# Kernel optimization log

Measured on AMD Instinct MI355X. Metric: run time of the kernel, lower is better.

The kernel has to match this reference:

```python
import jax, jax.numpy as jnp
import numpy as np

H = 4
HD = 32
C = 128
NU = 40000
NI = 40000
E = 200000


def _linear(x, W, b):
    # torch Linear: y = x @ W.T + b, W is [out, in]
    return x @ W.T + b


def _counts_in(query, sorted_keys):
    l = jnp.searchsorted(sorted_keys, query, side='left')
    r = jnp.searchsorted(sorted_keys, query, side='right')
    return (r - l).astype(jnp.float32)


def _segment_softmax(scores, seg, n):
    # scores: [E, H], seg: [E] destination ids
    m = jax.ops.segment_max(scores, seg, num_segments=n)
    m = jnp.where(jnp.isfinite(m), m, 0.0)
    e = jnp.exp(scores - m[seg])
    z = jax.ops.segment_sum(e, seg, num_segments=n)
    return e / z[seg]


def _deg_count(idx, n):
    return jnp.zeros((n,), jnp.float32).at[idx].add(1.0)


def _layernorm(x):
    mu = x.mean(-1, keepdims=True)
    var = ((x - mu) ** 2).mean(-1, keepdims=True)
    return (x - mu) / jnp.sqrt(var + 1e-5)


def _relation(x_src, x_dst, src, dst, t_src, t_dst,
              Wq, bq, Wk, bk, Wv, bv, Wo, bo,
              head_bias, beta, tau_raw, gamma, delta,
              counts, recips, n_dst):
    Q = _linear(x_dst, Wq, bq).reshape(-1, H, HD)
    K = _linear(x_src, Wk, bk).reshape(-1, H, HD)
    V = _linear(x_src, Wv, bv).reshape(-1, H, HD)
    Qe, Ke, Ve = Q[dst], K[src], V[src]                      # [E, H, HD]
    scores = (Qe * Ke).sum(-1) / jnp.sqrt(jnp.float32(HD))   # [E, H]
    scores = scores + head_bias
    dt = jnp.abs(t_dst[dst] - t_src[src]) + 1e-6
    tau = jax.nn.softplus(tau_raw) + 1e-6
    scores = scores + (-jnp.log1p(dt / tau))[:, None] * beta
    scores = scores + jnp.log1p(counts)[:, None] * gamma
    scores = scores + recips[:, None] * delta
    w = _segment_softmax(scores, dst, n_dst)                 # [E, H]
    out_e = (Ve * w[:, :, None]).reshape(-1, C)
    out_e = _linear(out_e, Wo, bo)
    return jnp.zeros((n_dst, C), x_dst.dtype).at[dst].add(out_e)


def setup_inputs() -> dict:
    key = jax.random.key(0)
    ks = jax.random.split(key, 20)
    inp = {
        'x_user': jax.random.normal(ks[0], (NU, C), jnp.float32),
        'x_item': jax.random.normal(ks[1], (NI, C), jnp.float32),
        't_user': jax.random.uniform(ks[2], (NU,), jnp.float32) * 100.0,
        't_item': jax.random.uniform(ks[3], (NI,), jnp.float32) * 100.0,
        'edge_index_ui': jax.random.randint(ks[4], (2, E), 0, NU, jnp.int32),
        'edge_index_iu': jax.random.randint(ks[5], (2, E), 0, NI, jnp.int32),
        'Wq': jax.random.normal(ks[6], (C, C), jnp.float32) * 0.05,
        'bq': jax.random.normal(ks[7], (C,), jnp.float32) * 0.05,
        'Wk': jax.random.normal(ks[8], (C, C), jnp.float32) * 0.05,
        'bk': jax.random.normal(ks[9], (C,), jnp.float32) * 0.05,
        'Wv': jax.random.normal(ks[10], (C, C), jnp.float32) * 0.05,
        'bv': jax.random.normal(ks[11], (C,), jnp.float32) * 0.05,
        'Wo': jax.random.normal(ks[12], (C, C), jnp.float32) * 0.05,
        'bo': jax.random.normal(ks[13], (C,), jnp.float32) * 0.05,
        'rel_head_bias': jax.random.normal(ks[14], (2, H), jnp.float32) * 0.1,
        'time_beta': jax.random.normal(ks[15], (2, H), jnp.float32) * 0.1,
        'time_tau_raw': jax.random.normal(ks[16], (2,), jnp.float32),
        'gamma_multirel': jax.random.normal(ks[17], (2, H), jnp.float32) * 0.1,
        'delta_recip': jax.random.normal(ks[18], (2, H), jnp.float32) * 0.1,
    }
    return inp


def reference(x_user, x_item, t_user, t_item, edge_index_ui, edge_index_iu,
              Wq, bq, Wk, bk, Wv, bv, Wo, bo,
              rel_head_bias, time_beta, time_tau_raw, gamma_multirel, delta_recip):
    su, du = edge_index_ui[0], edge_index_ui[1]   # user -> item
    si, di = edge_index_iu[0], edge_index_iu[1]   # item -> user
    # multirel counts (pair multiplicity - 1) and reciprocity flags, per relation
    pid_ui = su * NI + du            # (user,item) pair ids (fits int32: NU*NI < 2^31)
    pid_iu = si * NU + di            # (item,user) pair ids
    rev_for_ui = di * NI + si        # reversed pairs of iu edges in (user,item) space
    rev_for_iu = du * NU + su        # reversed pairs of ui edges in (item,user) space
    counts_ui = _counts_in(pid_ui, jnp.sort(pid_ui)) - 1.0
    counts_iu = _counts_in(pid_iu, jnp.sort(pid_iu)) - 1.0
    recips_ui = (_counts_in(pid_ui, jnp.sort(rev_for_ui)) > 0).astype(jnp.float32)
    recips_iu = (_counts_in(pid_iu, jnp.sort(rev_for_iu)) > 0).astype(jnp.float32)

    out_item = _relation(x_user, x_item, su, du, t_user, t_item,
                         Wq, bq, Wk, bk, Wv, bv, Wo, bo,
                         rel_head_bias[0], time_beta[0], time_tau_raw[0],
                         gamma_multirel[0], delta_recip[0], counts_ui, recips_ui, NI)
    out_user = _relation(x_item, x_user, si, di, t_item, t_user,
                         Wq, bq, Wk, bk, Wv, bv, Wo, bo,
                         rel_head_bias[1], time_beta[1], time_tau_raw[1],
                         gamma_multirel[1], delta_recip[1], counts_iu, recips_iu, NU)
    # degree centrality bias: total (in + out) degree added to every channel
    deg_user = _deg_count(su, NU) + _deg_count(di, NU)
    deg_item = _deg_count(du, NI) + _deg_count(si, NI)
    out_user = out_user + deg_user[:, None]
    out_item = out_item + deg_item[:, None]
    return _layernorm(out_user + x_user), _layernorm(out_item + x_item)
```

## Files before the change

kernel.cpp:

```cpp
#include <hip/hip_runtime.h>
#include <math.h>

constexpr int kH  = 4;
constexpr int kHD = 32;
constexpr int kC  = 128;
constexpr int kNU = 40000;
constexpr int kNI = 40000;
constexpr int kE  = 200000;
constexpr int kNT = kNU + kNI;
constexpr int kSB = (kNT + 1023) / 1024;
constexpr int kTilesPerSide = kNU / 16;
constexpr int kTiles = kNT / 16;
constexpr int kGemmBlocks  = 768;
constexpr int kTableBlocks = 1536;
constexpr int kFusedBlocks = 2304;

#define DEV_INLINE __device__ __forceinline__

typedef short bf16x8 __attribute__((ext_vector_type(8)));
typedef float f32x4  __attribute__((ext_vector_type(4)));
typedef uint32_t u32x4 __attribute__((ext_vector_type(4)));
typedef unsigned long long u64;

DEV_INLINE unsigned short f2bf(float f) {
  uint32_t u = __float_as_uint(f);
  u += 0x7fffu + ((u >> 16) & 1u);
  return (unsigned short)(u >> 16);
}

DEV_INLINE float bflo(uint32_t u) { return __uint_as_float(u << 16); }
DEV_INLINE float bfhi(uint32_t u) { return __uint_as_float(u & 0xffff0000u); }

DEV_INLINE int swz(int row, int elem) {
  return (elem & 7) | (((elem >> 3) ^ (row & 7)) << 3);
}

DEV_INLINE int rpf(const int* __restrict__ rp, const int* __restrict__ boff, int i) {
  return rp[i] + boff[i >> 10];
}

__global__ void cast4w_bf16(const float* __restrict__ w0, const float* __restrict__ w1,
                            const float* __restrict__ w2, const float* __restrict__ w3,
                            unsigned short* __restrict__ o0, unsigned short* __restrict__ o1,
                            unsigned short* __restrict__ o2, unsigned short* __restrict__ o3) {
  int i = blockIdx.x * blockDim.x + threadIdx.x;
  int m = i >> 12, j = i & 4095;
  const float* in = (m == 0) ? w0 : (m == 1) ? w1 : (m == 2) ? w2 : w3;
  unsigned short* out = (m == 0) ? o0 : (m == 1) ? o1 : (m == 2) ? o2 : o3;
  float4 v = ((const float4*)in)[j];
  ushort4 o = {f2bf(v.x), f2bf(v.y), f2bf(v.z), f2bf(v.w)};
  ((ushort4*)out)[j] = o;
}

__global__ __launch_bounds__(256, 3) void qkv_build(
    const float* __restrict__ Xu, const float* __restrict__ Xi,
    const unsigned short* __restrict__ Wq, const unsigned short* __restrict__ Wk,
    const unsigned short* __restrict__ Wv,
    const float* __restrict__ bq, const float* __restrict__ bk,
    const float* __restrict__ bv,
    unsigned short* __restrict__ Qu, unsigned short* __restrict__ Ku,
    unsigned short* __restrict__ Vu,
    unsigned short* __restrict__ Qi, unsigned short* __restrict__ Ki,
    unsigned short* __restrict__ Vi,
    const int* __restrict__ du, const int* __restrict__ di,
    int* __restrict__ deg_all, int* __restrict__ pos_all) {
  __shared__ unsigned short sx[16 * kC];
  __shared__ unsigned short sr[3 * 16 * kC];
  const int bid = blockIdx.x;
  const int tid = threadIdx.x;

  if (bid % 3 != 1) {
    const int tb = (bid / 3) * 2 + ((bid % 3) ? 1 : 0);
    for (int t = tb * 256 + tid; t < 2 * kE; t += kTableBlocks * 256) {
      if (t < kE) {
        pos_all[t] = atomicAdd(&deg_all[du[t]], 1);
      } else {
        pos_all[t] = atomicAdd(&deg_all[kNI + di[t - kE]], 1);
      }
    }
    return;
  }

  const int gb   = bid / 3;
  const int wave = tid >> 6;
  const int lane = tid & 63;
  const int mr   = lane & 15;
  const int quad = lane >> 4;
  const int ct0  = wave * 2;
  const int srow = tid >> 4;
  const int schk = tid & 15;

  bf16x8 wf[3][2][4];
  {
    const unsigned short* Ws[3] = {Wq, Wk, Wv};
#pragma unroll
    for (int m = 0; m < 3; ++m)
#pragma unroll
      for (int c = 0; c < 2; ++c) {
        const unsigned short* wrow = Ws[m] + (size_t)((ct0 + c) * 16 + mr) * kC + quad * 8;
#pragma unroll
        for (int kc = 0; kc < 4; ++kc) wf[m][c][kc] = *(const bf16x8*)(wrow + kc * 32);
      }
  }

  int tile = gb;
  float4 xa, xb;
  {
    const bool item = tile >= kTilesPerSide;
    const float* X = item ? Xi : Xu;
    const int base = (item ? tile - kTilesPerSide : tile) * 16;
    const float* xr = X + (size_t)(base + srow) * kC + schk * 8;
    xa = ((const float4*)xr)[0];
    xb = ((const float4*)xr)[1];
  }

  for (; tile < kTiles; tile += kGemmBlocks) {
    const bool item = tile >= kTilesPerSide;
    const int base = (item ? tile - kTilesPerSide : tile) * 16;

    {
      bf16x8 p;
      p[0] = (short)f2bf(xa.x); p[1] = (short)f2bf(xa.y);
      p[2] = (short)f2bf(xa.z); p[3] = (short)f2bf(xa.w);
      p[4] = (short)f2bf(xb.x); p[5] = (short)f2bf(xb.y);
      p[6] = (short)f2bf(xb.z); p[7] = (short)f2bf(xb.w);
      *(bf16x8*)(sx + srow * kC + ((schk ^ (srow & 7)) << 3)) = p;
    }
    __syncthreads();

    bf16x8 b[4];
#pragma unroll
    for (int kc = 0; kc < 4; ++kc)
      b[kc] = *(const bf16x8*)(sx + mr * kC + (((quad + kc * 4) ^ (mr & 7)) << 3));

    int ntile = tile + kGemmBlocks;
    if (ntile < kTiles) {
      const bool nit = ntile >= kTilesPerSide;
      const float* X = nit ? Xi : Xu;
      const int nbase = (nit ? ntile - kTilesPerSide : ntile) * 16;
      const float* xr = X + (size_t)(nbase + srow) * kC + schk * 8;
      xa = ((const float4*)xr)[0];
      xb = ((const float4*)xr)[1];
    }

    f32x4 acc[3][2];
#pragma unroll
    for (int m = 0; m < 3; ++m) {
      acc[m][0] = (f32x4){0.f, 0.f, 0.f, 0.f};
      acc[m][1] = (f32x4){0.f, 0.f, 0.f, 0.f};
    }
#pragma unroll
    for (int kc = 0; kc < 4; ++kc)
#pragma unroll
      for (int m = 0; m < 3; ++m)
#pragma unroll
        for (int c = 0; c < 2; ++c)
          acc[m][c] = __builtin_amdgcn_mfma_f32_16x16x32_bf16(wf[m][c][kc], b[kc], acc[m][c], 0, 0, 0);

    const float* bs[3] = {bq, bk, bv};
#pragma unroll
    for (int m = 0; m < 3; ++m)
#pragma unroll
      for (int c = 0; c < 2; ++c) {
        int c0 = (ct0 + c) * 16 + quad * 4;
        float4 bb = *(const float4*)(bs[m] + c0);
        uint2 p;
        p.x = (uint32_t)f2bf(acc[m][c][0] + bb.x) | ((uint32_t)f2bf(acc[m][c][1] + bb.y) << 16);
        p.y = (uint32_t)f2bf(acc[m][c][2] + bb.z) | ((uint32_t)f2bf(acc[m][c][3] + bb.w) << 16);
        *(uint2*)(sr + (m * 16 + mr) * kC + swz(mr, c0)) = p;
      }
    __syncthreads();

    {
      unsigned short* Os[3] = {item ? Qi : Qu, item ? Ki : Ku, item ? Vi : Vu};
      const int el = (schk ^ (srow & 7)) << 3;
#pragma unroll
      for (int m = 0; m < 3; ++m) {
        bf16x8 v = *(const bf16x8*)(sr + (m * 16 + srow) * kC + el);
        *(bf16x8*)(Os[m] + (size_t)(base + srow) * kC + schk * 8) = v;
      }
    }
  }
}

__global__ __launch_bounds__(256) void scan1(const int* __restrict__ in,
                                             int* __restrict__ out,
                                             int* __restrict__ bsum, int n) {
  __shared__ int sh[256];
  const int t = threadIdx.x;
  const int base = blockIdx.x * 1024 + t * 4;
  int4 v = {0, 0, 0, 0};
  if (base + 3 < n) {
    v = *(const int4*)(in + base);
  } else {
    if (base + 0 < n) v.x = in[base + 0];
    if (base + 1 < n) v.y = in[base + 1];
    if (base + 2 < n) v.z = in[base + 2];
    if (base + 3 < n) v.w = in[base + 3];
  }
  int s = v.x + v.y + v.z + v.w;
  sh[t] = s;
  __syncthreads();
  int val = s;
  for (int off = 1; off < 256; off <<= 1) {
    int add = (t >= off) ? sh[t - off] : 0;
    __syncthreads();
    val += add;
    sh[t] = val;
    __syncthreads();
  }
  int excl = val - s;
  if (base + 0 < n) out[base + 0] = excl;
  if (base + 1 < n) out[base + 1] = excl + v.x;
  if (base + 2 < n) out[base + 2] = excl + v.x + v.y;
  if (base + 3 < n) out[base + 3] = excl + v.x + v.y + v.z;
  if (t == 255) bsum[blockIdx.x] = val;
}

__global__ __launch_bounds__(128) void scan2(const int* __restrict__ bsum,
                                             int* __restrict__ boff,
                                             int* __restrict__ rp_tail, int nb) {
  __shared__ int sh[128];
  const int t = threadIdx.x;
  int v = (t < nb) ? bsum[t] : 0;
  sh[t] = v;
  __syncthreads();
  int val = v;
  for (int off = 1; off < 128; off <<= 1) {
    int add = (t >= off) ? sh[t - off] : 0;
    __syncthreads();
    val += add;
    sh[t] = val;
    __syncthreads();
  }
  if (t < nb) boff[t] = val - v;
  if (t == nb - 1) *rp_tail = v;
}

__global__ void scatter_pk(const int* __restrict__ su, const int* __restrict__ du,
                           const int* __restrict__ si, const int* __restrict__ di,
                           const int* __restrict__ rp_all, const int* __restrict__ boff,
                           const int* __restrict__ pos_all,
                           u64* __restrict__ el_all) {
  int t = blockIdx.x * blockDim.x + threadIdx.x;
  if (t >= 2 * kE) return;
  int e, s, dg;
  if (t < kE) { e = t;       s = su[e]; dg = du[e]; }
  else        { e = t - kE;  s = si[e]; dg = kNI + di[e]; }
  el_all[rpf(rp_all, boff, dg) + pos_all[t]] = (u64)(uint32_t)e | ((u64)(uint32_t)s << 32);
}

__global__ void bias_csr(const int* __restrict__ su, const int* __restrict__ du,
                         const int* __restrict__ si, const int* __restrict__ di,
                         const float* __restrict__ t_user, const float* __restrict__ t_item,
                         const int* __restrict__ rp_all, const int* __restrict__ boff,
                         const u64* __restrict__ el_all,
                         const float* __restrict__ hb, const float* __restrict__ beta,
                         const float* __restrict__ taur,
                         const float* __restrict__ gamma, const float* __restrict__ delta,
                         float4* __restrict__ bias_ui, float4* __restrict__ bias_iu) {
  int t = blockIdx.x * blockDim.x + threadIdx.x;
  if (t >= 2 * kE) return;
  const int rel = (t >= kE) ? 1 : 0;
  const int e = rel ? t - kE : t;
  int s, d; float ts, td; int dg, rg;
  if (rel == 0) {
    s = su[e]; d = du[e]; ts = t_user[s]; td = t_item[d];
    dg = d;
    rg = kNI + s;
  } else {
    s = si[e]; d = di[e]; ts = t_item[s]; td = t_user[d];
    dg = kNI + d;
    rg = s;
  }
  int b0 = rpf(rp_all, boff, dg), b1 = rpf(rp_all, boff, dg + 1);
  int cnt = 0;
  for (int p = b0; p < b1; ++p) cnt += ((int)(el_all[p] >> 32) == s);
  int r0 = rpf(rp_all, boff, rg), r1 = rpf(rp_all, boff, rg + 1);
  int rcp = 0;
  for (int p = r0; p < r1; ++p) rcp |= ((int)(el_all[p] >> 32) == d);

  float cntv = (float)(cnt - 1);
  float rec  = (float)rcp;
  float dt   = fabsf(td - ts) + 1e-6f;
  float tau  = log1pf(expf(taur[rel])) + 1e-6f;
  float tterm = -log1pf(dt / tau);
  float lc    = log1pf(cntv);
  const float* hp = hb + rel * kH;
  const float* bp = beta + rel * kH;
  const float* gp = gamma + rel * kH;
  const float* dp = delta + rel * kH;
  const float kL2E = 1.4426950408889634f;
  float4 b;
  b.x = (hp[0] + bp[0] * tterm + gp[0] * lc + dp[0] * rec) * kL2E;
  b.y = (hp[1] + bp[1] * tterm + gp[1] * lc + dp[1] * rec) * kL2E;
  b.z = (hp[2] + bp[2] * tterm + gp[2] * lc + dp[2] * rec) * kL2E;
  b.w = (hp[3] + bp[3] * tterm + gp[3] * lc + dp[3] * rec) * kL2E;
  (rel ? bias_iu : bias_ui)[e] = b;
}

__global__ __launch_bounds__(256) void attn_agg(
    const int* __restrict__ rp_all, const int* __restrict__ boff,
    const u64* __restrict__ el_all,
    const unsigned short* __restrict__ Qi, const unsigned short* __restrict__ Ku,
    const unsigned short* __restrict__ Vu,
    const unsigned short* __restrict__ Qu, const unsigned short* __restrict__ Ki,
    const unsigned short* __restrict__ Vi,
    const float* __restrict__ bias_ui, const float* __restrict__ bias_iu,
    unsigned short* __restrict__ h_ui, unsigned short* __restrict__ h_iu) {
  const int tid = threadIdx.x;
  const int sub = tid & 15;
  const int h   = sub >> 2;
  const int ch0 = h * kHD + (sub & 3) * 8;
  const int g = blockIdx.x * 16 + (tid >> 4);
  if (g >= kNT) return;
  const bool isU = g >= kNI;
  const int n = isU ? g - kNI : g;
  const unsigned short* Q = isU ? Qu : Qi;
  const unsigned short* K = isU ? Ki : Ku;
  const unsigned short* V = isU ? Vi : Vu;
  const float* bias = isU ? bias_iu : bias_ui;
  unsigned short* out = isU ? h_iu : h_ui;

  const int beg = rpf(rp_all, boff, g), end = rpf(rp_all, boff, g + 1);
  const float kScaleL2E = 1.4426950408889634f * 0.17677669529663687f;

  float qf[8];
  {
    u32x4 qv = *(const u32x4*)(Q + (size_t)n * kC + ch0);
#pragma unroll
    for (int w = 0; w < 4; ++w) { qf[2 * w] = bflo(qv[w]); qf[2 * w + 1] = bfhi(qv[w]); }
  }

  float z = 0.f;
  float acc[8] = {0.f, 0.f, 0.f, 0.f, 0.f, 0.f, 0.f, 0.f};

  int e0 = 0, s0 = 0;
  if (beg < end) { u64 pk = el_all[beg]; e0 = (int)pk; s0 = (int)(pk >> 32); }
  u32x4 k0 = *(const u32x4*)(K + (size_t)s0 * kC + ch0);
  u32x4 v0 = *(const u32x4*)(V + (size_t)s0 * kC + ch0);
  float b0 = bias[e0 * 4 + h];

  for (int p = beg; p < end; ++p) {
    int e1 = 0, s1 = 0;
    if (p + 1 < end) { u64 pk = el_all[p + 1]; e1 = (int)pk; s1 = (int)(pk >> 32); }
    u32x4 k1 = *(const u32x4*)(K + (size_t)s1 * kC + ch0);
    u32x4 v1 = *(const u32x4*)(V + (size_t)s1 * kC + ch0);
    float b1 = bias[e1 * 4 + h];

    float d0 = qf[0] * bflo(k0[0]);
    float d1 = qf[1] * bfhi(k0[0]);
    d0 = fmaf(qf[2], bflo(k0[1]), d0);
    d1 = fmaf(qf[3], bfhi(k0[1]), d1);
    d0 = fmaf(qf[4], bflo(k0[2]), d0);
    d1 = fmaf(qf[5], bfhi(k0[2]), d1);
    d0 = fmaf(qf[6], bflo(k0[3]), d0);
    d1 = fmaf(qf[7], bfhi(k0[3]), d1);
    float dsc = d0 + d1;
    dsc += __shfl_xor(dsc, 1);
    dsc += __shfl_xor(dsc, 2);
    float wgt = __builtin_amdgcn_exp2f(fmaf(dsc, kScaleL2E, b0));
    z += wgt;
#pragma unroll
    for (int w = 0; w < 4; ++w) {
      acc[2 * w]     = fmaf(bflo(v0[w]), wgt, acc[2 * w]);
      acc[2 * w + 1] = fmaf(bfhi(v0[w]), wgt, acc[2 * w + 1]);
    }
    k0 = k1; v0 = v1; b0 = b1;
  }

  const float zi = (end > beg) ? 1.0f / z : 0.0f;
  bf16x8 o;
#pragma unroll
  for (int j = 0; j < 8; ++j) o[j] = (short)f2bf(acc[j] * zi);
  *(bf16x8*)(out + (size_t)n * kC + ch0) = o;
}

__global__ __launch_bounds__(256, 4) void wo_ln(
    const unsigned short* __restrict__ Hiu, const unsigned short* __restrict__ Hui,
    const unsigned short* __restrict__ Wo,
    const float* __restrict__ Xu, const float* __restrict__ Xi,
    const int* __restrict__ degU, const int* __restrict__ degI,
    const float* __restrict__ bo, float* __restrict__ out) {
  __shared__ unsigned short sh_h[16 * kC];
  __shared__ float sh_p[64 * 2];
  const int tid  = threadIdx.x;
  const int wave = tid >> 6;
  const int lane = tid & 63;
  const int mr   = lane & 15;
  const int quad = lane >> 4;
  const int ct0  = wave * 2;
  const int srow = tid >> 4;
  const int schk = tid & 15;

  bf16x8 wf[2][4];
#pragma unroll
  for (int c = 0; c < 2; ++c) {
    const unsigned short* wrow = Wo + (size_t)((ct0 + c) * 16 + mr) * kC + quad * 8;
#pragma unroll
    for (int kc = 0; kc < 4; ++kc) wf[c][kc] = *(const bf16x8*)(wrow + kc * 32);
  }
  float4 bb[2];
  bb[0] = *(const float4*)(bo + ct0 * 16 + quad * 4);
  bb[1] = *(const float4*)(bo + (ct0 + 1) * 16 + quad * 4);

  int tile = blockIdx.x;
  bf16x8 hv;
  {
    const bool item = tile >= kTilesPerSide;
    const unsigned short* Hs = item ? Hui : Hiu;
    const int base = (item ? tile - kTilesPerSide : tile) * 16;
    hv = *(const bf16x8*)(Hs + (size_t)(base + srow) * kC + schk * 8);
  }

  for (; tile < kTiles; tile += gridDim.x) {
    const bool item = tile >= kTilesPerSide;
    const int base = (item ? tile - kTilesPerSide : tile) * 16;

    *(bf16x8*)(sh_h + srow * kC + ((schk ^ (srow & 7)) << 3)) = hv;
    __syncthreads();

    bf16x8 b[4];
#pragma unroll
    for (int kc = 0; kc < 4; ++kc)
      b[kc] = *(const bf16x8*)(sh_h + mr * kC + (((quad + kc * 4) ^ (mr & 7)) << 3));

    int ntile = tile + gridDim.x;
    if (ntile < kTiles) {
      const bool nit = ntile >= kTilesPerSide;
      const unsigned short* Hs = nit ? Hui : Hiu;
      const int nbase = (nit ? ntile - kTilesPerSide : ntile) * 16;
      hv = *(const bf16x8*)(Hs + (size_t)(nbase + srow) * kC + schk * 8);
    }

    f32x4 acc[2];
    acc[0] = (f32x4){0.f, 0.f, 0.f, 0.f};
    acc[1] = (f32x4){0.f, 0.f, 0.f, 0.f};
#pragma unroll
    for (int kc = 0; kc < 4; ++kc) {
      acc[0] = __builtin_amdgcn_mfma_f32_16x16x32_bf16(wf[0][kc], b[kc], acc[0], 0, 0, 0);
      acc[1] = __builtin_amdgcn_mfma_f32_16x16x32_bf16(wf[1][kc], b[kc], acc[1], 0, 0, 0);
    }

    const int n = base + mr;
    const float* Xs = item ? Xi : Xu;
    const float fdg = (float)(item ? degI[n] : degU[n]);
    float y[8], s1 = 0.f, s2 = 0.f;
#pragma unroll
    for (int c = 0; c < 2; ++c) {
      int c0 = (ct0 + c) * 16 + quad * 4;
      float4 xv = *(const float4*)(Xs + (size_t)n * kC + c0);
      y[c * 4 + 0] = acc[c][0] + xv.x + fdg * bb[c].x;
      y[c * 4 + 1] = acc[c][1] + xv.y + fdg * bb[c].y;
      y[c * 4 + 2] = acc[c][2] + xv.z + fdg * bb[c].z;
      y[c * 4 + 3] = acc[c][3] + xv.w + fdg * bb[c].w;
#pragma unroll
      for (int j = 0; j < 4; ++j) {
        s1 += y[c * 4 + j];
        s2 += y[c * 4 + j] * y[c * 4 + j];
      }
    }
    s1 += __shfl_xor(s1, 16); s2 += __shfl_xor(s2, 16);
    s1 += __shfl_xor(s1, 32); s2 += __shfl_xor(s2, 32);
    if (quad == 0) {
      sh_p[(wave * 16 + mr) * 2]     = s1;
      sh_p[(wave * 16 + mr) * 2 + 1] = s2;
    }
    __syncthreads();
    float t1 = 0.f, t2 = 0.f;
#pragma unroll
    for (int ww = 0; ww < 4; ++ww) {
      t1 += sh_p[(ww * 16 + mr) * 2];
      t2 += sh_p[(ww * 16 + mr) * 2 + 1];
    }
    float mu   = t1 * (1.0f / 128.0f);
    float var  = t2 * (1.0f / 128.0f) - mu * mu;
    float rstd = rsqrtf(fmaxf(var, 0.0f) + 1e-5f);
    float* op = out + (item ? (size_t)kNU * kC : (size_t)0) + (size_t)n * kC;
#pragma unroll
    for (int c = 0; c < 2; ++c) {
      int c0 = (ct0 + c) * 16 + quad * 4;
      float4 o = {(y[c * 4 + 0] - mu) * rstd, (y[c * 4 + 1] - mu) * rstd,
                  (y[c * 4 + 2] - mu) * rstd, (y[c * 4 + 3] - mu) * rstd};
      *(float4*)(op + c0) = o;
    }
  }
}

extern "C" void kernel_launch(void* const* d_in, const int* in_sizes, int n_in,
                              void* d_out, int out_size, void* d_ws, size_t ws_size,
                              hipStream_t stream) {
  const float* x_user = (const float*)d_in[0];
  const float* x_item = (const float*)d_in[1];
  const float* t_user = (const float*)d_in[2];
  const float* t_item = (const float*)d_in[3];
  const int*   eui    = (const int*)d_in[4];
  const int*   eiu    = (const int*)d_in[5];
  const float* Wq = (const float*)d_in[6];
  const float* bq = (const float*)d_in[7];
  const float* Wk = (const float*)d_in[8];
  const float* bk = (const float*)d_in[9];
  const float* Wv = (const float*)d_in[10];
  const float* bv = (const float*)d_in[11];
  const float* Wo = (const float*)d_in[12];
  const float* bo = (const float*)d_in[13];
  const float* hb    = (const float*)d_in[14];
  const float* beta  = (const float*)d_in[15];
  const float* taur  = (const float*)d_in[16];
  const float* gamma = (const float*)d_in[17];
  const float* delta = (const float*)d_in[18];

  const int* su = eui;       const int* du = eui + kE;
  const int* si = eiu;       const int* di = eiu + kE;

  float* w = (float*)d_ws;
  size_t o = 0;
  unsigned short* qu_b = (unsigned short*)(w + o); o += (size_t)kNU * kC / 2;
  unsigned short* ku_b = (unsigned short*)(w + o); o += (size_t)kNU * kC / 2;
  unsigned short* vu_b = (unsigned short*)(w + o); o += (size_t)kNU * kC / 2;
  unsigned short* qi_b = (unsigned short*)(w + o); o += (size_t)kNI * kC / 2;
  unsigned short* ki_b = (unsigned short*)(w + o); o += (size_t)kNI * kC / 2;
  unsigned short* vi_b = (unsigned short*)(w + o); o += (size_t)kNI * kC / 2;
  unsigned short* h_ui = (unsigned short*)(w + o); o += (size_t)kNI * kC / 2;
  unsigned short* h_iu = (unsigned short*)(w + o); o += (size_t)kNU * kC / 2;
  unsigned short* wq_b = (unsigned short*)(w + o); o += kC * kC / 2;
  unsigned short* wk_b = (unsigned short*)(w + o); o += kC * kC / 2;
  unsigned short* wv_b = (unsigned short*)(w + o); o += kC * kC / 2;
  unsigned short* wo_b = (unsigned short*)(w + o); o += kC * kC / 2;
  float* zero_base = w + o;
  int* deg_all = (int*)(w + o); o += kNT;
  size_t zero_bytes = (size_t)((w + o) - zero_base) * sizeof(float);
  float* bias_ui = w + o; o += (size_t)kE * kH;
  float* bias_iu = w + o; o += (size_t)kE * kH;
  int* rp_all  = (int*)(w + o); o += kNT + 1;
  int* bsum    = (int*)(w + o); o += kSB;
  int* boff    = (int*)(w + o); o += kSB;
  o = (o + 1) & ~(size_t)1;
  u64* el_all  = (u64*)(w + o); o += (size_t)2 * kE * 2;
  int* pos_all = (int*)h_ui;

  hipMemsetAsync(zero_base, 0, zero_bytes, stream);

  dim3 b256(256);
  cast4w_bf16<<<(4 * kC * kC / 4) / 256, b256, 0, stream>>>(Wq, Wk, Wv, Wo,
                                                            wq_b, wk_b, wv_b, wo_b);

  qkv_build<<<kFusedBlocks, b256, 0, stream>>>(
      x_user, x_item, wq_b, wk_b, wv_b, bq, bk, bv,
      qu_b, ku_b, vu_b, qi_b, ki_b, vi_b,
      du, di, deg_all, pos_all);

  scan1<<<kSB, b256, 0, stream>>>(deg_all, rp_all, bsum, kNT);
  scan2<<<1, dim3(128), 0, stream>>>(bsum, boff, rp_all + kNT, kSB);

  int g2E = (2 * kE + 255) / 256;
  scatter_pk<<<g2E, b256, 0, stream>>>(su, du, si, di, rp_all, boff, pos_all, el_all);

  bias_csr<<<g2E, b256, 0, stream>>>(su, du, si, di, t_user, t_item,
                                     rp_all, boff, el_all,
                                     hb, beta, taur, gamma, delta,
                                     (float4*)bias_ui, (float4*)bias_iu);

  attn_agg<<<(kNT + 15) / 16, b256, 0, stream>>>(rp_all, boff, el_all,
                                                 qi_b, ku_b, vu_b, qu_b, ki_b, vi_b,
                                                 bias_ui, bias_iu, h_ui, h_iu);

  wo_ln<<<768, b256, 0, stream>>>(h_iu, h_ui, wo_b, x_user, x_item,
                                  deg_all + kNI, deg_all, bo, (float*)d_out);
}
```

Baseline: 255.0 us.

## Fuse attention aggregation with Wo projection and layernorm epilogue

Merges the per-destination attention aggregation kernel and the Wo projection plus residual plus layernorm kernel into one kernel. Each block aggregates 16 destination rows into shared memory, then runs the MFMA projection and layernorm on that tile directly. This removes the bf16 round trip of the aggregated tensors through global memory and one kernel launch. In exchange, the persistent-loop prefetch of the old projection kernel is dropped, and the Wo fragments are reloaded per block. The scatter positions buffer now gets its own workspace slot because the aggregated-output buffer it used to alias no longer exists.

```diff
diff --git a/kernel.cpp b/kernel.cpp
--- a/kernel.cpp
+++ b/kernel.cpp
@@ -299,7 +299,7 @@
   (rel ? bias_iu : bias_ui)[e] = b;
 }
 
-__global__ __launch_bounds__(256) void attn_agg(
+__global__ __launch_bounds__(256, 4) void attn_wo_ln(
     const int* __restrict__ rp_all, const int* __restrict__ boff,
     const u64* __restrict__ el_all,
     const unsigned short* __restrict__ Qi, const unsigned short* __restrict__ Ku,
@@ -307,27 +307,31 @@
     const unsigned short* __restrict__ Qu, const unsigned short* __restrict__ Ki,
     const unsigned short* __restrict__ Vi,
     const float* __restrict__ bias_ui, const float* __restrict__ bias_iu,
-    unsigned short* __restrict__ h_ui, unsigned short* __restrict__ h_iu) {
+    const unsigned short* __restrict__ Wo,
+    const float* __restrict__ Xu, const float* __restrict__ Xi,
+    const int* __restrict__ deg_all,
+    const float* __restrict__ bo, float* __restrict__ out) {
+  __shared__ unsigned short sh_h[16 * kC];
+  __shared__ float sh_p[64 * 2];
   const int tid = threadIdx.x;
   const int sub = tid & 15;
-  const int h   = sub >> 2;
-  const int ch0 = h * kHD + (sub & 3) * 8;
-  const int g = blockIdx.x * 16 + (tid >> 4);
-  if (g >= kNT) return;
+  const int hh  = sub >> 2;
+  const int ch0 = hh * kHD + (sub & 3) * 8;
+  const int grp = tid >> 4;
+  const int g = blockIdx.x * 16 + grp;
   const bool isU = g >= kNI;
-  const int n = isU ? g - kNI : g;
+  const int n1 = isU ? g - kNI : g;
   const unsigned short* Q = isU ? Qu : Qi;
   const unsigned short* K = isU ? Ki : Ku;
   const unsigned short* V = isU ? Vi : Vu;
   const float* bias = isU ? bias_iu : bias_ui;
-  unsigned short* out = isU ? h_iu : h_ui;
 
   const int beg = rpf(rp_all, boff, g), end = rpf(rp_all, boff, g + 1);
   const float kScaleL2E = 1.4426950408889634f * 0.17677669529663687f;
 
   float qf[8];
   {
-    u32x4 qv = *(const u32x4*)(Q + (size_t)n * kC + ch0);
+    u32x4 qv = *(const u32x4*)(Q + (size_t)n1 * kC + ch0);
 #pragma unroll
     for (int w = 0; w < 4; ++w) { qf[2 * w] = bflo(qv[w]); qf[2 * w + 1] = bfhi(qv[w]); }
   }
@@ -339,14 +343,14 @@
   if (beg < end) { u64 pk = el_all[beg]; e0 = (int)pk; s0 = (int)(pk >> 32); }
   u32x4 k0 = *(const u32x4*)(K + (size_t)s0 * kC + ch0);
   u32x4 v0 = *(const u32x4*)(V + (size_t)s0 * kC + ch0);
-  float b0 = bias[e0 * 4 + h];
+  float b0 = bias[e0 * 4 + hh];
 
   for (int p = beg; p < end; ++p) {
     int e1 = 0, s1 = 0;
     if (p + 1 < end) { u64 pk = el_all[p + 1]; e1 = (int)pk; s1 = (int)(pk >> 32); }
     u32x4 k1 = *(const u32x4*)(K + (size_t)s1 * kC + ch0);
     u32x4 v1 = *(const u32x4*)(V + (size_t)s1 * kC + ch0);
-    float b1 = bias[e1 * 4 + h];
+    float b1 = bias[e1 * 4 + hh];
 
     float d0 = qf[0] * bflo(k0[0]);
     float d1 = qf[1] * bfhi(k0[0]);
@@ -369,29 +373,23 @@
     k0 = k1; v0 = v1; b0 = b1;
   }
 
-  const float zi = (end > beg) ? 1.0f / z : 0.0f;
-  bf16x8 o;
-#pragma unroll
-  for (int j = 0; j < 8; ++j) o[j] = (short)f2bf(acc[j] * zi);
-  *(bf16x8*)(out + (size_t)n * kC + ch0) = o;
-}
-
-__global__ __launch_bounds__(256, 4) void wo_ln(
-    const unsigned short* __restrict__ Hiu, const unsigned short* __restrict__ Hui,
-    const unsigned short* __restrict__ Wo,
-    const float* __restrict__ Xu, const float* __restrict__ Xi,
-    const int* __restrict__ degU, const int* __restrict__ degI,
-    const float* __restrict__ bo, float* __restrict__ out) {
-  __shared__ unsigned short sh_h[16 * kC];
-  __shared__ float sh_p[64 * 2];
-  const int tid  = threadIdx.x;
+  {
+    const float zi = (end > beg) ? 1.0f / z : 0.0f;
+    bf16x8 o;
+#pragma unroll
+    for (int j = 0; j < 8; ++j) o[j] = (short)f2bf(acc[j] * zi);
+    const int chunk = ch0 >> 3;
+    *(bf16x8*)(sh_h + grp * kC + ((chunk ^ (grp & 7)) << 3)) = o;
+  }
+  __syncthreads();
+
+  const bool itemDst = blockIdx.x < kTilesPerSide;
+  const int base = (itemDst ? blockIdx.x : blockIdx.x - kTilesPerSide) * 16;
   const int wave = tid >> 6;
   const int lane = tid & 63;
   const int mr   = lane & 15;
   const int quad = lane >> 4;
   const int ct0  = wave * 2;
-  const int srow = tid >> 4;
-  const int schk = tid & 15;
 
   bf16x8 wf[2][4];
 #pragma unroll
@@ -404,86 +402,62 @@
   bb[0] = *(const float4*)(bo + ct0 * 16 + quad * 4);
   bb[1] = *(const float4*)(bo + (ct0 + 1) * 16 + quad * 4);
 
-  int tile = blockIdx.x;
-  bf16x8 hv;
-  {
-    const bool item = tile >= kTilesPerSide;
-    const unsigned short* Hs = item ? Hui : Hiu;
-    const int base = (item ? tile - kTilesPerSide : tile) * 16;
-    hv = *(const bf16x8*)(Hs + (size_t)(base + srow) * kC + schk * 8);
-  }
-
-  for (; tile < kTiles; tile += gridDim.x) {
-    const bool item = tile >= kTilesPerSide;
-    const int base = (item ? tile - kTilesPerSide : tile) * 16;
-
-    *(bf16x8*)(sh_h + srow * kC + ((schk ^ (srow & 7)) << 3)) = hv;
-    __syncthreads();
-
-    bf16x8 b[4];
-#pragma unroll
-    for (int kc = 0; kc < 4; ++kc)
-      b[kc] = *(const bf16x8*)(sh_h + mr * kC + (((quad + kc * 4) ^ (mr & 7)) << 3));
-
-    int ntile = tile + gridDim.x;
-    if (ntile < kTiles) {
-      const bool nit = ntile >= kTilesPerSide;
-      const unsigned short* Hs = nit ? Hui : Hiu;
-      const int nbase = (nit ? ntile - kTilesPerSide : ntile) * 16;
-      hv = *(const bf16x8*)(Hs + (size_t)(nbase + srow) * kC + schk * 8);
-    }
-
-    f32x4 acc[2];
-    acc[0] = (f32x4){0.f, 0.f, 0.f, 0.f};
-    acc[1] = (f32x4){0.f, 0.f, 0.f, 0.f};
-#pragma unroll
-    for (int kc = 0; kc < 4; ++kc) {
-      acc[0] = __builtin_amdgcn_mfma_f32_16x16x32_bf16(wf[0][kc], b[kc], acc[0], 0, 0, 0);
-      acc[1] = __builtin_amdgcn_mfma_f32_16x16x32_bf16(wf[1][kc], b[kc], acc[1], 0, 0, 0);
-    }
-
-    const int n = base + mr;
-    const float* Xs = item ? Xi : Xu;
-    const float fdg = (float)(item ? degI[n] : degU[n]);
-    float y[8], s1 = 0.f, s2 = 0.f;
-#pragma unroll
-    for (int c = 0; c < 2; ++c) {
-      int c0 = (ct0 + c) * 16 + quad * 4;
-      float4 xv = *(const float4*)(Xs + (size_t)n * kC + c0);
-      y[c * 4 + 0] = acc[c][0] + xv.x + fdg * bb[c].x;
-      y[c * 4 + 1] = acc[c][1] + xv.y + fdg * bb[c].y;
-      y[c * 4 + 2] = acc[c][2] + xv.z + fdg * bb[c].z;
-      y[c * 4 + 3] = acc[c][3] + xv.w + fdg * bb[c].w;
-#pragma unroll
-      for (int j = 0; j < 4; ++j) {
-        s1 += y[c * 4 + j];
-        s2 += y[c * 4 + j] * y[c * 4 + j];
-      }
-    }
-    s1 += __shfl_xor(s1, 16); s2 += __shfl_xor(s2, 16);
-    s1 += __shfl_xor(s1, 32); s2 += __shfl_xor(s2, 32);
-    if (quad == 0) {
-      sh_p[(wave * 16 + mr) * 2]     = s1;
-      sh_p[(wave * 16 + mr) * 2 + 1] = s2;
-    }
-    __syncthreads();
-    float t1 = 0.f, t2 = 0.f;
-#pragma unroll
-    for (int ww = 0; ww < 4; ++ww) {
-      t1 += sh_p[(ww * 16 + mr) * 2];
-      t2 += sh_p[(ww * 16 + mr) * 2 + 1];
-    }
-    float mu   = t1 * (1.0f / 128.0f);
-    float var  = t2 * (1.0f / 128.0f) - mu * mu;
-    float rstd = rsqrtf(fmaxf(var, 0.0f) + 1e-5f);
-    float* op = out + (item ? (size_t)kNU * kC : (size_t)0) + (size_t)n * kC;
-#pragma unroll
-    for (int c = 0; c < 2; ++c) {
-      int c0 = (ct0 + c) * 16 + quad * 4;
-      float4 o = {(y[c * 4 + 0] - mu) * rstd, (y[c * 4 + 1] - mu) * rstd,
-                  (y[c * 4 + 2] - mu) * rstd, (y[c * 4 + 3] - mu) * rstd};
-      *(float4*)(op + c0) = o;
-    }
+  bf16x8 b[4];
+#pragma unroll
+  for (int kc = 0; kc < 4; ++kc)
+    b[kc] = *(const bf16x8*)(sh_h + mr * kC + (((quad + kc * 4) ^ (mr & 7)) << 3));
+
+  f32x4 wacc[2];
+  wacc[0] = (f32x4){0.f, 0.f, 0.f, 0.f};
+  wacc[1] = (f32x4){0.f, 0.f, 0.f, 0.f};
+#pragma unroll
+  for (int kc = 0; kc < 4; ++kc) {
+    wacc[0] = __builtin_amdgcn_mfma_f32_16x16x32_bf16(wf[0][kc], b[kc], wacc[0], 0, 0, 0);
+    wacc[1] = __builtin_amdgcn_mfma_f32_16x16x32_bf16(wf[1][kc], b[kc], wacc[1], 0, 0, 0);
+  }
+
+  const int n = base + mr;
+  const float* Xs = itemDst ? Xi : Xu;
+  const int* deg = itemDst ? deg_all : (deg_all + kNI);
+  const float fdg = (float)deg[n];
+  float y[8], s1 = 0.f, s2 = 0.f;
+#pragma unroll
+  for (int c = 0; c < 2; ++c) {
+    int c0 = (ct0 + c) * 16 + quad * 4;
+    float4 xv = *(const float4*)(Xs + (size_t)n * kC + c0);
+    y[c * 4 + 0] = wacc[c][0] + xv.x + fdg * bb[c].x;
+    y[c * 4 + 1] = wacc[c][1] + xv.y + fdg * bb[c].y;
+    y[c * 4 + 2] = wacc[c][2] + xv.z + fdg * bb[c].z;
+    y[c * 4 + 3] = wacc[c][3] + xv.w + fdg * bb[c].w;
+#pragma unroll
+    for (int j = 0; j < 4; ++j) {
+      s1 += y[c * 4 + j];
+      s2 += y[c * 4 + j] * y[c * 4 + j];
+    }
+  }
+  s1 += __shfl_xor(s1, 16); s2 += __shfl_xor(s2, 16);
+  s1 += __shfl_xor(s1, 32); s2 += __shfl_xor(s2, 32);
+  if (quad == 0) {
+    sh_p[(wave * 16 + mr) * 2]     = s1;
+    sh_p[(wave * 16 + mr) * 2 + 1] = s2;
+  }
+  __syncthreads();
+  float t1 = 0.f, t2 = 0.f;
+#pragma unroll
+  for (int ww = 0; ww < 4; ++ww) {
+    t1 += sh_p[(ww * 16 + mr) * 2];
+    t2 += sh_p[(ww * 16 + mr) * 2 + 1];
+  }
+  float mu   = t1 * (1.0f / 128.0f);
+  float var  = t2 * (1.0f / 128.0f) - mu * mu;
+  float rstd = rsqrtf(fmaxf(var, 0.0f) + 1e-5f);
+  float* op = out + (itemDst ? (size_t)kNU * kC : (size_t)0) + (size_t)n * kC;
+#pragma unroll
+  for (int c = 0; c < 2; ++c) {
+    int c0 = (ct0 + c) * 16 + quad * 4;
+    float4 o = {(y[c * 4 + 0] - mu) * rstd, (y[c * 4 + 1] - mu) * rstd,
+                (y[c * 4 + 2] - mu) * rstd, (y[c * 4 + 3] - mu) * rstd};
+    *(float4*)(op + c0) = o;
   }
 }
 
@@ -521,8 +495,6 @@
   unsigned short* qi_b = (unsigned short*)(w + o); o += (size_t)kNI * kC / 2;
   unsigned short* ki_b = (unsigned short*)(w + o); o += (size_t)kNI * kC / 2;
   unsigned short* vi_b = (unsigned short*)(w + o); o += (size_t)kNI * kC / 2;
-  unsigned short* h_ui = (unsigned short*)(w + o); o += (size_t)kNI * kC / 2;
-  unsigned short* h_iu = (unsigned short*)(w + o); o += (size_t)kNU * kC / 2;
   unsigned short* wq_b = (unsigned short*)(w + o); o += kC * kC / 2;
   unsigned short* wk_b = (unsigned short*)(w + o); o += kC * kC / 2;
   unsigned short* wv_b = (unsigned short*)(w + o); o += kC * kC / 2;
@@ -535,9 +507,9 @@
   int* rp_all  = (int*)(w + o); o += kNT + 1;
   int* bsum    = (int*)(w + o); o += kSB;
   int* boff    = (int*)(w + o); o += kSB;
+  int* pos_all = (int*)(w + o); o += 2 * kE;
   o = (o + 1) & ~(size_t)1;
   u64* el_all  = (u64*)(w + o); o += (size_t)2 * kE * 2;
-  int* pos_all = (int*)h_ui;
 
   hipMemsetAsync(zero_base, 0, zero_bytes, stream);
 
@@ -561,10 +533,9 @@
                                      hb, beta, taur, gamma, delta,
                                      (float4*)bias_ui, (float4*)bias_iu);
 
-  attn_agg<<<(kNT + 15) / 16, b256, 0, stream>>>(rp_all, boff, el_all,
-                                                 qi_b, ku_b, vu_b, qu_b, ki_b, vi_b,
-                                                 bias_ui, bias_iu, h_ui, h_iu);
-
-  wo_ln<<<768, b256, 0, stream>>>(h_iu, h_ui, wo_b, x_user, x_item,
-                                  deg_all + kNI, deg_all, bo, (float*)d_out);
-}
+  attn_wo_ln<<<kTiles, b256, 0, stream>>>(rp_all, boff, el_all,
+                                          qi_b, ku_b, vu_b, qu_b, ki_b, vi_b,
+                                          bias_ui, bias_iu,
+                                          wo_b, x_user, x_item, deg_all,
+                                          bo, (float*)d_out);
+}
```

After: 258.6 us. No clear change (+1.4%).
